# Kernel optimization log

Hardware: AMD Instinct MI355X
Metric: run time of the kernel (lower is better)

## Reference

```python
import jax, jax.numpy as jnp
import numpy as np

C = 1.0      # base manifold curvature (Lorentz c)
C_E = 1.0    # expert manifold curvature (all experts init to c=1.0)
K = 1        # n_activated_experts (top-k)
SCALE = 2.0  # LResNet scale for shared-expert combine
EPS = 1e-8


def _lorentz_swiglu(x, W1, W3, W2, c_mid, c_out, prescale):
    """LorentzExpert / LorentzFeedForward: SwiGLU on space coords with Lorentz time lift.
    x: [T, D] (full Lorentz vector). W1,W3: [I-1, D]; W2: [D-1, I]. Returns [T, D]."""
    if prescale:
        x = x * np.float32(np.sqrt(C_E / C))  # x * sqrt(c_expert / c)
    s1 = jax.nn.silu(x @ W1.T)                 # [T, I-1] w1(x, return_space=True)
    s3 = x @ W3.T                              # [T, I-1] w3(x, return_space=True)
    sp = s1 * s3                               # gated space part
    t = jnp.sqrt(jnp.clip((sp * sp).sum(-1, keepdims=True) + c_mid, EPS))
    h = jnp.concatenate([t, sp], axis=-1)      # [T, I] point on expert manifold
    o = h @ W2.T                               # [T, D-1] w2 space output
    ot = jnp.sqrt(jnp.clip((o * o).sum(-1, keepdims=True) + c_out, EPS))
    return jnp.concatenate([ot, o], axis=-1)   # [T, D] on base manifold


def setup_inputs() -> dict:
    key = jax.random.key(0)
    ks = jax.random.split(key, 9)
    T, D, E, I = 2048, 1024, 8, 1024
    x = jax.random.normal(ks[0], (T, D), jnp.float32)
    gate_w = jax.random.normal(ks[1], (E, D - 1), jnp.float32) / np.sqrt(D - 1)
    gate_b = jax.random.normal(ks[2], (E,), jnp.float32) * 0.01
    W1 = jax.random.normal(ks[3], (E, I - 1, D), jnp.float32) / np.sqrt(D)
    W3 = jax.random.normal(ks[4], (E, I - 1, D), jnp.float32) / np.sqrt(D)
    W2 = jax.random.normal(ks[5], (E, D - 1, I), jnp.float32) / np.sqrt(I)
    Ws1 = jax.random.normal(ks[6], (I - 1, D), jnp.float32) / np.sqrt(D)
    Ws3 = jax.random.normal(ks[7], (I - 1, D), jnp.float32) / np.sqrt(D)
    Ws2 = jax.random.normal(ks[8], (D - 1, I), jnp.float32) / np.sqrt(I)
    return {"x": x, "gate_w": gate_w, "gate_b": gate_b, "W1": W1, "W3": W3,
            "W2": W2, "Ws1": Ws1, "Ws3": Ws3, "Ws2": Ws2}


def reference(x, gate_w, gate_b, W1, W3, W2, Ws1, Ws3, Ws2):
    T, D = x.shape
    E = gate_w.shape[0]
    # ---- Gate (softmax scoring, n_groups == 1, route_scale == 1.0) ----
    logits = x[:, 1:] @ gate_w.T                                    # [T, E]
    scores = jax.nn.softmax(logits.astype(jnp.float32), axis=-1)
    biased = scores + gate_b                                        # bias only affects routing
    _, idx = jax.lax.top_k(biased, K)                               # [T, K]
    weights = jnp.take_along_axis(scores, idx, axis=-1).astype(x.dtype)  # [T, K]
    # dense per-token expert gate weights [T, E]
    oh = jax.nn.one_hot(idx, E, dtype=x.dtype)                      # [T, K, E]
    gw = (oh * weights[..., None]).sum(axis=1)                      # [T, E]
    # ---- y init: project(zeros) -> [sqrt(c), 0, ..., 0] ----
    y0 = jnp.concatenate([jnp.full((T, 1), np.sqrt(C), x.dtype),
                          jnp.zeros((T, D - 1), x.dtype)], axis=-1)
    # ---- routed experts (dense reference: every expert on every token, masked combine) ----
    e_out = jax.vmap(lambda w1, w3, w2: _lorentz_swiglu(x, w1, w3, w2, C_E, C, True))(W1, W3, W2)  # [E, T, D]
    y = y0 + jnp.einsum('te,etd->td', gw, e_out)
    # ---- shared expert (LorentzFeedForward, stays on base manifold) ----
    z = _lorentz_swiglu(x, Ws1, Ws3, Ws2, C, C, False)
    # ---- LResNet weighted sum: normalize (z + scale*y) back to manifold ----
    comb = z + SCALE * y
    li = (comb[:, 1:] ** 2).sum(-1, keepdims=True) - comb[:, :1] ** 2  # Lorentz inner <comb,comb>
    out = np.float32(np.sqrt(C)) * comb / jnp.sqrt(jnp.clip(jnp.abs(li), EPS))
    return out
```

## Files before the change

### kernel.cpp

```cpp
#include <hip/hip_runtime.h>

typedef __bf16 bf16;
typedef __attribute__((ext_vector_type(8))) __bf16 bf16x8;
typedef __attribute__((ext_vector_type(4))) float floatx4;

#define TOK 2048
#define DD  1024
#define NE  8
#define LDA 40

__device__ __forceinline__ uint4 pack_bf8(float4 a, float4 b) {
  union { bf16 h[8]; uint4 u; } p;
  p.h[0] = (bf16)a.x; p.h[1] = (bf16)a.y; p.h[2] = (bf16)a.z; p.h[3] = (bf16)a.w;
  p.h[4] = (bf16)b.x; p.h[5] = (bf16)b.y; p.h[6] = (bf16)b.z; p.h[7] = (bf16)b.w;
  return p.u;
}

__global__ __launch_bounds__(256) void gate_cvt_kernel(
    const float* __restrict__ x, const float* __restrict__ gate_w,
    const float* __restrict__ gate_b, bf16* __restrict__ x_bf,
    int* __restrict__ eidx, float* __restrict__ ewgt)
{
  const int t = blockIdx.x, tid = threadIdx.x;
  const float4 v = ((const float4*)(x + (size_t)t * DD))[tid];
  union { bf16 h[4]; uint2 u; } pk;
  pk.h[0] = (bf16)v.x; pk.h[1] = (bf16)v.y; pk.h[2] = (bf16)v.z; pk.h[3] = (bf16)v.w;
  ((uint2*)(x_bf + (size_t)t * DD))[tid] = pk.u;

  float acc[NE];
#pragma unroll
  for (int e = 0; e < NE; ++e) acc[e] = 0.f;
  const float vv[4] = {v.x, v.y, v.z, v.w};
#pragma unroll
  for (int i = 0; i < 4; ++i) {
    const int d = tid * 4 + i;
    if (d >= 1) {
#pragma unroll
      for (int e = 0; e < NE; ++e) acc[e] += vv[i] * gate_w[e * (DD - 1) + d - 1];
    }
  }
#pragma unroll
  for (int off = 32; off > 0; off >>= 1) {
#pragma unroll
    for (int e = 0; e < NE; ++e) acc[e] += __shfl_down(acc[e], off);
  }
  __shared__ float red[4][NE];
  const int wid = tid >> 6, lane = tid & 63;
  if (lane == 0) {
#pragma unroll
    for (int e = 0; e < NE; ++e) red[wid][e] = acc[e];
  }
  __syncthreads();
  if (tid == 0) {
    float lg[NE];
#pragma unroll
    for (int e = 0; e < NE; ++e) lg[e] = red[0][e] + red[1][e] + red[2][e] + red[3][e];
    float m = lg[0];
    for (int e = 1; e < NE; ++e) m = fmaxf(m, lg[e]);
    float ex[NE], s = 0.f;
    for (int e = 0; e < NE; ++e) { ex[e] = expf(lg[e] - m); s += ex[e]; }
    const float inv = 1.f / s;
    int best = 0; float bb = ex[0] * inv + gate_b[0];
    for (int e = 1; e < NE; ++e) {
      const float b = ex[e] * inv + gate_b[e];
      if (b > bb) { bb = b; best = e; }
    }
    eidx[t] = best;
    ewgt[t] = ex[best] * inv;
  }
}

__global__ __launch_bounds__(256) void route_kernel(
    const int* __restrict__ eidx, int* __restrict__ perm,
    int* __restrict__ pos_of, int* __restrict__ seg_base)
{
  __shared__ int cnt[NE], off[NE], bas[NE + 1];
  const int tid = threadIdx.x;
  if (tid < NE) cnt[tid] = 0;
  __syncthreads();
  for (int t = tid; t < TOK; t += 256) atomicAdd(&cnt[eidx[t]], 1);
  __syncthreads();
  if (tid == 0) {
    int run = 0;
    for (int e = 0; e < NE; ++e) { bas[e] = run; off[e] = run; run += cnt[e]; }
    bas[NE] = run;
  }
  __syncthreads();
  for (int t = tid; t < TOK; t += 256) {
    const int e = eidx[t];
    const int p = atomicAdd(&off[e], 1);
    perm[p] = t;
    pos_of[t] = p;
  }
  if (tid <= NE) seg_base[tid] = bas[tid];
}

__global__ __launch_bounds__(256) void mlp1_kernel(
    const bf16* __restrict__ x_bf,
    const float* __restrict__ W1, const float* __restrict__ W3,
    const float* __restrict__ Ws1, const float* __restrict__ Ws3,
    const int* __restrict__ perm, const int* __restrict__ seg_base,
    bf16* __restrict__ h_r, bf16* __restrict__ h_s,
    float* __restrict__ ss_r, float* __restrict__ ss_z)
{
  const int nt = blockIdx.x;
  const int mslot = blockIdx.y;
  const int tid = threadIdx.x;
  int base, cnt, row0;
  const float *w1p, *w3p;
  const int* permp;
  bf16* hbuf;
  float* ssbuf;
  if (mslot < 128) {
    const int e = mslot >> 4;
    base = seg_base[e];
    cnt  = seg_base[e + 1] - base;
    row0 = (mslot & 15) * 128;
    if (row0 >= cnt) return;
    w1p = W1 + (size_t)e * 1023 * 1024;
    w3p = W3 + (size_t)e * 1023 * 1024;
    permp = perm; hbuf = h_r; ssbuf = ss_r;
  } else {
    base = 0; cnt = TOK; row0 = (mslot - 128) * 128;
    w1p = Ws1; w3p = Ws3;
    permp = nullptr; hbuf = h_s; ssbuf = ss_z;
  }
  const int n0 = nt * 64;

  __shared__ __align__(16) bf16 As[128 * LDA];
  __shared__ __align__(16) bf16 B1s[64 * LDA];
  __shared__ __align__(16) bf16 B3s[64 * LDA];
  __shared__ int toks[128];

  if (tid < 128) {
    int r = row0 + tid;
    if (r >= cnt) r = cnt - 1;
    toks[tid] = permp ? permp[base + r] : r;
  }
  __syncthreads();

  const int arow = tid >> 1, acol = (tid & 1) * 16;
  const bf16* aptr = x_bf + (size_t)toks[arow] * DD + acol;
  bf16* const alds = As + arow * LDA + acol;

  const int brow = tid >> 2, bcol = (tid & 3) * 8;
  int bn = n0 + brow; if (bn > 1022) bn = 1022;
  const float* b1ptr = w1p + (size_t)bn * 1024 + bcol;
  const float* b3ptr = w3p + (size_t)bn * 1024 + bcol;
  bf16* const b1lds = B1s + brow * LDA + bcol;
  bf16* const b3lds = B3s + brow * LDA + bcol;

  const int wid = tid >> 6, lane = tid & 63;
  const int wr = (wid >> 1) * 64, wc = (wid & 1) * 32;
  const int lrow = lane & 15, quad = lane >> 4;

  const floatx4 fz = {0.f, 0.f, 0.f, 0.f};
  floatx4 acc1[4][2], acc3[4][2];
#pragma unroll
  for (int mi = 0; mi < 4; ++mi)
#pragma unroll
    for (int ni = 0; ni < 2; ++ni) { acc1[mi][ni] = fz; acc3[mi][ni] = fz; }

  uint4  a0  = *(const uint4*)(aptr);
  uint4  a1  = *(const uint4*)(aptr + 8);
  float4 f10 = *(const float4*)(b1ptr);
  float4 f11 = *(const float4*)(b1ptr + 4);
  float4 f30 = *(const float4*)(b3ptr);
  float4 f31 = *(const float4*)(b3ptr + 4);

  for (int k0 = 0; k0 < 1024; k0 += 32) {
    __syncthreads();
    *(uint4*)alds       = a0;
    *(uint4*)(alds + 8) = a1;
    *(uint4*)b1lds = pack_bf8(f10, f11);
    *(uint4*)b3lds = pack_bf8(f30, f31);
    __syncthreads();
    const int kn = (k0 + 32 < 1024) ? (k0 + 32) : 0;
    a0  = *(const uint4*)(aptr + kn);
    a1  = *(const uint4*)(aptr + kn + 8);
    f10 = *(const float4*)(b1ptr + kn);
    f11 = *(const float4*)(b1ptr + kn + 4);
    f30 = *(const float4*)(b3ptr + kn);
    f31 = *(const float4*)(b3ptr + kn + 4);

    bf16x8 af[4], b1f[2], b3f[2];
#pragma unroll
    for (int mi = 0; mi < 4; ++mi)
      af[mi] = *(const bf16x8*)(As + (wr + mi * 16 + lrow) * LDA + quad * 8);
#pragma unroll
    for (int ni = 0; ni < 2; ++ni) {
      b1f[ni] = *(const bf16x8*)(B1s + (wc + ni * 16 + lrow) * LDA + quad * 8);
      b3f[ni] = *(const bf16x8*)(B3s + (wc + ni * 16 + lrow) * LDA + quad * 8);
    }
#pragma unroll
    for (int mi = 0; mi < 4; ++mi)
#pragma unroll
      for (int ni = 0; ni < 2; ++ni) {
        acc1[mi][ni] = __builtin_amdgcn_mfma_f32_16x16x32_bf16(af[mi], b1f[ni], acc1[mi][ni], 0, 0, 0);
        acc3[mi][ni] = __builtin_amdgcn_mfma_f32_16x16x32_bf16(af[mi], b3f[ni], acc3[mi][ni], 0, 0, 0);
      }
  }

  const int mbase = base + row0;
#pragma unroll
  for (int mi = 0; mi < 4; ++mi) {
#pragma unroll
    for (int r = 0; r < 4; ++r) {
      const int row = wr + mi * 16 + quad * 4 + r;
      const bool rowok = (row0 + row) < cnt;
      float ssum = 0.f;
#pragma unroll
      for (int ni = 0; ni < 2; ++ni) {
        const float s1 = acc1[mi][ni][r];
        const float s3 = acc3[mi][ni][r];
        const float sp = (s1 / (1.f + __expf(-s1))) * s3;
        const int n = n0 + wc + ni * 16 + lrow;
        if (rowok && n < 1023) {
          hbuf[(size_t)(mbase + row) * 1024 + 1 + n] = (bf16)sp;
          ssum += sp * sp;
        }
      }
      ssum += __shfl_xor(ssum, 1);
      ssum += __shfl_xor(ssum, 2);
      ssum += __shfl_xor(ssum, 4);
      ssum += __shfl_xor(ssum, 8);
      if (lrow == 0 && rowok) atomicAdd(ssbuf + mbase + row, ssum);
    }
  }
}

__global__ __launch_bounds__(256) void finalize_t_kernel(
    const float* __restrict__ ss_r, const float* __restrict__ ss_z,
    bf16* __restrict__ h_r, bf16* __restrict__ h_s)
{
  const int i = blockIdx.x * 256 + threadIdx.x;
  if (i < TOK) {
    h_r[(size_t)i * 1024] = (bf16)sqrtf(ss_r[i] + 1.0f);
    h_s[(size_t)i * 1024] = (bf16)sqrtf(ss_z[i] + 1.0f);
  }
}

__global__ __launch_bounds__(256) void mlp2_kernel(
    const bf16* __restrict__ h_r, const bf16* __restrict__ h_s,
    const float* __restrict__ W2, const float* __restrict__ Ws2,
    const int* __restrict__ seg_base,
    float* __restrict__ o_r, float* __restrict__ o_s,
    float* __restrict__ ss_or, float* __restrict__ ss_oz)
{
  const int nt = blockIdx.x;
  const int mslot = blockIdx.y;
  const int tid = threadIdx.x;
  int base, cnt, row0;
  const float* wp;
  const bf16* abuf;
  float *obuf, *ssbuf;
  if (mslot < 128) {
    const int e = mslot >> 4;
    base = seg_base[e];
    cnt  = seg_base[e + 1] - base;
    row0 = (mslot & 15) * 128;
    if (row0 >= cnt) return;
    wp = W2 + (size_t)e * 1023 * 1024;
    abuf = h_r; obuf = o_r; ssbuf = ss_or;
  } else {
    base = 0; cnt = TOK; row0 = (mslot - 128) * 128;
    wp = Ws2; abuf = h_s; obuf = o_s; ssbuf = ss_oz;
  }
  const int n0 = nt * 128;

  __shared__ __align__(16) bf16 As[128 * LDA];
  __shared__ __align__(16) bf16 Bs[128 * LDA];

  const int arow = tid >> 1, acol = (tid & 1) * 16;
  int ar = row0 + arow; if (ar >= cnt) ar = cnt - 1;
  const bf16* aptr = abuf + (size_t)(base + ar) * 1024 + acol;
  bf16* const alds = As + arow * LDA + acol;

  const int brow = tid >> 1, bcol = (tid & 1) * 16;
  int bn = n0 + brow; if (bn > 1022) bn = 1022;
  const float* bptr = wp + (size_t)bn * 1024 + bcol;
  bf16* const blds = Bs + brow * LDA + bcol;

  const int wid = tid >> 6, lane = tid & 63;
  const int wr = (wid >> 1) * 64, wc = (wid & 1) * 64;
  const int lrow = lane & 15, quad = lane >> 4;

  const floatx4 fz = {0.f, 0.f, 0.f, 0.f};
  floatx4 acc[4][4];
#pragma unroll
  for (int mi = 0; mi < 4; ++mi)
#pragma unroll
    for (int ni = 0; ni < 4; ++ni) acc[mi][ni] = fz;

  uint4  a0 = *(const uint4*)(aptr);
  uint4  a1 = *(const uint4*)(aptr + 8);
  float4 f0 = *(const float4*)(bptr);
  float4 f1 = *(const float4*)(bptr + 4);
  float4 f2 = *(const float4*)(bptr + 8);
  float4 f3 = *(const float4*)(bptr + 12);

  for (int k0 = 0; k0 < 1024; k0 += 32) {
    __syncthreads();
    *(uint4*)alds       = a0;
    *(uint4*)(alds + 8) = a1;
    *(uint4*)blds       = pack_bf8(f0, f1);
    *(uint4*)(blds + 8) = pack_bf8(f2, f3);
    __syncthreads();
    const int kn = (k0 + 32 < 1024) ? (k0 + 32) : 0;
    a0 = *(const uint4*)(aptr + kn);
    a1 = *(const uint4*)(aptr + kn + 8);
    f0 = *(const float4*)(bptr + kn);
    f1 = *(const float4*)(bptr + kn + 4);
    f2 = *(const float4*)(bptr + kn + 8);
    f3 = *(const float4*)(bptr + kn + 12);

    bf16x8 af[4], bf_[4];
#pragma unroll
    for (int mi = 0; mi < 4; ++mi)
      af[mi] = *(const bf16x8*)(As + (wr + mi * 16 + lrow) * LDA + quad * 8);
#pragma unroll
    for (int ni = 0; ni < 4; ++ni)
      bf_[ni] = *(const bf16x8*)(Bs + (wc + ni * 16 + lrow) * LDA + quad * 8);
#pragma unroll
    for (int mi = 0; mi < 4; ++mi)
#pragma unroll
      for (int ni = 0; ni < 4; ++ni)
        acc[mi][ni] = __builtin_amdgcn_mfma_f32_16x16x32_bf16(af[mi], bf_[ni], acc[mi][ni], 0, 0, 0);
  }

  const int mbase = base + row0;
#pragma unroll
  for (int mi = 0; mi < 4; ++mi) {
#pragma unroll
    for (int r = 0; r < 4; ++r) {
      const int row = wr + mi * 16 + quad * 4 + r;
      const bool rowok = (row0 + row) < cnt;
      float ssum = 0.f;
#pragma unroll
      for (int ni = 0; ni < 4; ++ni) {
        const float v = acc[mi][ni][r];
        const int n = n0 + wc + ni * 16 + lrow;
        if (rowok && n < 1023) {
          obuf[(size_t)(mbase + row) * 1024 + n] = v;
          ssum += v * v;
        }
      }
      ssum += __shfl_xor(ssum, 1);
      ssum += __shfl_xor(ssum, 2);
      ssum += __shfl_xor(ssum, 4);
      ssum += __shfl_xor(ssum, 8);
      if (lrow == 0 && rowok) atomicAdd(ssbuf + mbase + row, ssum);
    }
  }
}

__global__ __launch_bounds__(256) void combine_kernel(
    const float* __restrict__ o_r, const float* __restrict__ o_s,
    const float* __restrict__ ss_or, const float* __restrict__ ss_oz,
    const int* __restrict__ pos_of, const float* __restrict__ wgt,
    float* __restrict__ out)
{
  const int t = blockIdx.x, tid = threadIdx.x;
  const int p = pos_of[t];
  const float w = wgt[t];
  const float4 oz = ((const float4*)(o_s + (size_t)t * 1024))[tid];
  const float4 oe = ((const float4*)(o_r + (size_t)p * 1024))[tid];
  const float tw = 2.f * w;
  float c0 = oz.x + tw * oe.x;
  float c1 = oz.y + tw * oe.y;
  float c2 = oz.z + tw * oe.z;
  float c3 = (tid == 255) ? 0.f : (oz.w + tw * oe.w);
  float ssum = c0 * c0 + c1 * c1 + c2 * c2 + c3 * c3;
#pragma unroll
  for (int off = 32; off > 0; off >>= 1) ssum += __shfl_down(ssum, off);
  __shared__ float rs[4];
  if ((tid & 63) == 0) rs[tid >> 6] = ssum;
  __syncthreads();
  const float space2 = rs[0] + rs[1] + rs[2] + rs[3];
  const float comb0 = sqrtf(ss_oz[t] + 1.f) + 2.f + 2.f * w * sqrtf(ss_or[p] + 1.f);
  const float li = space2 - comb0 * comb0;
  const float inv = 1.f / sqrtf(fmaxf(fabsf(li), 1e-8f));
  float* orow = out + (size_t)t * 1024;
  const int j = 1 + tid * 4;
  orow[j]     = c0 * inv;
  orow[j + 1] = c1 * inv;
  orow[j + 2] = c2 * inv;
  if (tid != 255) orow[j + 3] = c3 * inv;
  if (tid == 0) orow[0] = comb0 * inv;
}

extern "C" void kernel_launch(void* const* d_in, const int* in_sizes, int n_in,
                              void* d_out, int out_size, void* d_ws, size_t ws_size,
                              hipStream_t stream) {
  const float* x      = (const float*)d_in[0];
  const float* gate_w = (const float*)d_in[1];
  const float* gate_b = (const float*)d_in[2];
  const float* W1     = (const float*)d_in[3];
  const float* W3     = (const float*)d_in[4];
  const float* W2     = (const float*)d_in[5];
  const float* Ws1    = (const float*)d_in[6];
  const float* Ws3    = (const float*)d_in[7];
  const float* Ws2    = (const float*)d_in[8];
  float* out = (float*)d_out;

  char* ws = (char*)d_ws;
  size_t off = 0;
  auto alloc = [&](size_t bytes) {
    void* p = ws + off;
    off += (bytes + 255) & ~(size_t)255;
    return p;
  };
  bf16*  x_bf = (bf16*) alloc((size_t)TOK * 1024 * 2);
  bf16*  h_r  = (bf16*) alloc((size_t)TOK * 1024 * 2);
  bf16*  h_s  = (bf16*) alloc((size_t)TOK * 1024 * 2);
  float* o_r  = (float*)alloc((size_t)TOK * 1024 * 4);
  float* o_s  = (float*)alloc((size_t)TOK * 1024 * 4);
  float* ss   = (float*)alloc((size_t)4 * TOK * 4);
  int*   eidx = (int*)  alloc((size_t)TOK * 4);
  float* ewgt = (float*)alloc((size_t)TOK * 4);
  int*   perm = (int*)  alloc((size_t)TOK * 4);
  int*   posf = (int*)  alloc((size_t)TOK * 4);
  int*   segb = (int*)  alloc(64);

  float* ss_r  = ss;
  float* ss_z  = ss + TOK;
  float* ss_or = ss + 2 * TOK;
  float* ss_oz = ss + 3 * TOK;

  hipMemsetAsync(ss, 0, (size_t)4 * TOK * 4, stream);
  gate_cvt_kernel<<<TOK, 256, 0, stream>>>(x, gate_w, gate_b, x_bf, eidx, ewgt);
  route_kernel<<<1, 256, 0, stream>>>(eidx, perm, posf, segb);
  mlp1_kernel<<<dim3(16, 144), 256, 0, stream>>>(x_bf, W1, W3, Ws1, Ws3, perm, segb,
                                                 h_r, h_s, ss_r, ss_z);
  finalize_t_kernel<<<8, 256, 0, stream>>>(ss_r, ss_z, h_r, h_s);
  mlp2_kernel<<<dim3(8, 144), 256, 0, stream>>>(h_r, h_s, W2, Ws2, segb,
                                                o_r, o_s, ss_or, ss_oz);
  combine_kernel<<<TOK, 256, 0, stream>>>(o_r, o_s, ss_or, ss_oz, posf, ewgt, out);
}
```

Measured before the change: 278.6 us.

## Build compact per-expert work list and shrink GEMM tiles to 64 rows

New measurement: 285.1 us. +2.3%, slower.

```diff
diff --git a/kernel.cpp b/kernel.cpp
--- a/kernel.cpp
+++ b/kernel.cpp
@@ -8,6 +8,7 @@
 #define DD  1024
 #define NE  8
 #define LDA 40
+#define MAXSLOT 72
 
 __device__ __forceinline__ uint4 pack_bf8(float4 a, float4 b) {
   union { bf16 h[8]; uint4 u; } p;
@@ -72,7 +73,7 @@
 
 __global__ __launch_bounds__(256) void route_kernel(
     const int* __restrict__ eidx, int* __restrict__ perm,
-    int* __restrict__ pos_of, int* __restrict__ seg_base)
+    int* __restrict__ pos_of, int4* __restrict__ wl, int* __restrict__ wl_n)
 {
   __shared__ int cnt[NE], off[NE], bas[NE + 1];
   const int tid = threadIdx.x;
@@ -84,6 +85,14 @@
     int run = 0;
     for (int e = 0; e < NE; ++e) { bas[e] = run; off[e] = run; run += cnt[e]; }
     bas[NE] = run;
+    int n = 0;
+    for (int e = 0; e < NE; ++e)
+      for (int r0 = 0; r0 < cnt[e]; r0 += 64) {
+        int rows = cnt[e] - r0; if (rows > 64) rows = 64;
+        wl[n++] = make_int4(bas[e] + r0, rows, e, 0);
+      }
+    for (int r0 = 0; r0 < TOK; r0 += 64) wl[n++] = make_int4(r0, 64, NE, 0);
+    *wl_n = n;
   }
   __syncthreads();
   for (int t = tid; t < TOK; t += 256) {
@@ -92,54 +101,42 @@
     perm[p] = t;
     pos_of[t] = p;
   }
-  if (tid <= NE) seg_base[tid] = bas[tid];
 }
 
 __global__ __launch_bounds__(256) void mlp1_kernel(
     const bf16* __restrict__ x_bf,
     const float* __restrict__ W1, const float* __restrict__ W3,
     const float* __restrict__ Ws1, const float* __restrict__ Ws3,
-    const int* __restrict__ perm, const int* __restrict__ seg_base,
+    const int* __restrict__ perm, const int4* __restrict__ wl,
+    const int* __restrict__ wl_n,
     bf16* __restrict__ h_r, bf16* __restrict__ h_s,
     float* __restrict__ ss_r, float* __restrict__ ss_z)
 {
-  const int nt = blockIdx.x;
-  const int mslot = blockIdx.y;
+  const int bid = blockIdx.x;
+  const int slot = bid >> 4, nt = bid & 15;
+  if (slot >= *wl_n) return;
+  const int4 wle = wl[slot];
+  const int mbase = wle.x, rows = wle.y, eid = wle.z;
   const int tid = threadIdx.x;
-  int base, cnt, row0;
-  const float *w1p, *w3p;
-  const int* permp;
-  bf16* hbuf;
-  float* ssbuf;
-  if (mslot < 128) {
-    const int e = mslot >> 4;
-    base = seg_base[e];
-    cnt  = seg_base[e + 1] - base;
-    row0 = (mslot & 15) * 128;
-    if (row0 >= cnt) return;
-    w1p = W1 + (size_t)e * 1023 * 1024;
-    w3p = W3 + (size_t)e * 1023 * 1024;
-    permp = perm; hbuf = h_r; ssbuf = ss_r;
-  } else {
-    base = 0; cnt = TOK; row0 = (mslot - 128) * 128;
-    w1p = Ws1; w3p = Ws3;
-    permp = nullptr; hbuf = h_s; ssbuf = ss_z;
-  }
+  const bool routed = (eid < NE);
+  const float* w1p = routed ? W1 + (size_t)eid * 1023 * 1024 : Ws1;
+  const float* w3p = routed ? W3 + (size_t)eid * 1023 * 1024 : Ws3;
+  bf16* hbuf  = routed ? h_r : h_s;
+  float* ssbuf = routed ? ss_r : ss_z;
   const int n0 = nt * 64;
 
-  __shared__ __align__(16) bf16 As[128 * LDA];
+  __shared__ __align__(16) bf16 As[64 * LDA];
   __shared__ __align__(16) bf16 B1s[64 * LDA];
   __shared__ __align__(16) bf16 B3s[64 * LDA];
-  __shared__ int toks[128];
-
-  if (tid < 128) {
-    int r = row0 + tid;
-    if (r >= cnt) r = cnt - 1;
-    toks[tid] = permp ? permp[base + r] : r;
-  }
-  __syncthreads();
-
-  const int arow = tid >> 1, acol = (tid & 1) * 16;
+  __shared__ int toks[64];
+
+  if (tid < 64) {
+    int r = tid < rows ? tid : rows - 1;
+    toks[tid] = routed ? perm[mbase + r] : (mbase + r);
+  }
+  __syncthreads();
+
+  const int arow = tid >> 2, acol = (tid & 3) * 8;
   const bf16* aptr = x_bf + (size_t)toks[arow] * DD + acol;
   bf16* const alds = As + arow * LDA + acol;
 
@@ -151,18 +148,15 @@
   bf16* const b3lds = B3s + brow * LDA + bcol;
 
   const int wid = tid >> 6, lane = tid & 63;
-  const int wr = (wid >> 1) * 64, wc = (wid & 1) * 32;
+  const int wc = wid * 16;
   const int lrow = lane & 15, quad = lane >> 4;
 
   const floatx4 fz = {0.f, 0.f, 0.f, 0.f};
-  floatx4 acc1[4][2], acc3[4][2];
-#pragma unroll
-  for (int mi = 0; mi < 4; ++mi)
-#pragma unroll
-    for (int ni = 0; ni < 2; ++ni) { acc1[mi][ni] = fz; acc3[mi][ni] = fz; }
+  floatx4 acc1[4], acc3[4];
+#pragma unroll
+  for (int mi = 0; mi < 4; ++mi) { acc1[mi] = fz; acc3[mi] = fz; }
 
   uint4  a0  = *(const uint4*)(aptr);
-  uint4  a1  = *(const uint4*)(aptr + 8);
   float4 f10 = *(const float4*)(b1ptr);
   float4 f11 = *(const float4*)(b1ptr + 4);
   float4 f30 = *(const float4*)(b3ptr);
@@ -170,61 +164,47 @@
 
   for (int k0 = 0; k0 < 1024; k0 += 32) {
     __syncthreads();
-    *(uint4*)alds       = a0;
-    *(uint4*)(alds + 8) = a1;
+    *(uint4*)alds  = a0;
     *(uint4*)b1lds = pack_bf8(f10, f11);
     *(uint4*)b3lds = pack_bf8(f30, f31);
     __syncthreads();
     const int kn = (k0 + 32 < 1024) ? (k0 + 32) : 0;
     a0  = *(const uint4*)(aptr + kn);
-    a1  = *(const uint4*)(aptr + kn + 8);
     f10 = *(const float4*)(b1ptr + kn);
     f11 = *(const float4*)(b1ptr + kn + 4);
     f30 = *(const float4*)(b3ptr + kn);
     f31 = *(const float4*)(b3ptr + kn + 4);
 
-    bf16x8 af[4], b1f[2], b3f[2];
+    bf16x8 af[4], b1f, b3f;
 #pragma unroll
     for (int mi = 0; mi < 4; ++mi)
-      af[mi] = *(const bf16x8*)(As + (wr + mi * 16 + lrow) * LDA + quad * 8);
-#pragma unroll
-    for (int ni = 0; ni < 2; ++ni) {
-      b1f[ni] = *(const bf16x8*)(B1s + (wc + ni * 16 + lrow) * LDA + quad * 8);
-      b3f[ni] = *(const bf16x8*)(B3s + (wc + ni * 16 + lrow) * LDA + quad * 8);
-    }
-#pragma unroll
-    for (int mi = 0; mi < 4; ++mi)
-#pragma unroll
-      for (int ni = 0; ni < 2; ++ni) {
-        acc1[mi][ni] = __builtin_amdgcn_mfma_f32_16x16x32_bf16(af[mi], b1f[ni], acc1[mi][ni], 0, 0, 0);
-        acc3[mi][ni] = __builtin_amdgcn_mfma_f32_16x16x32_bf16(af[mi], b3f[ni], acc3[mi][ni], 0, 0, 0);
-      }
-  }
-
-  const int mbase = base + row0;
+      af[mi] = *(const bf16x8*)(As + (mi * 16 + lrow) * LDA + quad * 8);
+    b1f = *(const bf16x8*)(B1s + (wc + lrow) * LDA + quad * 8);
+    b3f = *(const bf16x8*)(B3s + (wc + lrow) * LDA + quad * 8);
+#pragma unroll
+    for (int mi = 0; mi < 4; ++mi) {
+      acc1[mi] = __builtin_amdgcn_mfma_f32_16x16x32_bf16(af[mi], b1f, acc1[mi], 0, 0, 0);
+      acc3[mi] = __builtin_amdgcn_mfma_f32_16x16x32_bf16(af[mi], b3f, acc3[mi], 0, 0, 0);
+    }
+  }
+
+  const int n = n0 + wc + lrow;
 #pragma unroll
   for (int mi = 0; mi < 4; ++mi) {
 #pragma unroll
     for (int r = 0; r < 4; ++r) {
-      const int row = wr + mi * 16 + quad * 4 + r;
-      const bool rowok = (row0 + row) < cnt;
-      float ssum = 0.f;
-#pragma unroll
-      for (int ni = 0; ni < 2; ++ni) {
-        const float s1 = acc1[mi][ni][r];
-        const float s3 = acc3[mi][ni][r];
-        const float sp = (s1 / (1.f + __expf(-s1))) * s3;
-        const int n = n0 + wc + ni * 16 + lrow;
-        if (rowok && n < 1023) {
-          hbuf[(size_t)(mbase + row) * 1024 + 1 + n] = (bf16)sp;
-          ssum += sp * sp;
-        }
-      }
+      const int row = mi * 16 + quad * 4 + r;
+      const bool ok = (row < rows) && (n < 1023);
+      const float s1 = acc1[mi][r];
+      const float s3 = acc3[mi][r];
+      const float sp = (s1 / (1.f + __expf(-s1))) * s3;
+      float ssum = ok ? sp * sp : 0.f;
+      if (ok) hbuf[(size_t)(mbase + row) * 1024 + 1 + n] = (bf16)sp;
       ssum += __shfl_xor(ssum, 1);
       ssum += __shfl_xor(ssum, 2);
       ssum += __shfl_xor(ssum, 4);
       ssum += __shfl_xor(ssum, 8);
-      if (lrow == 0 && rowok) atomicAdd(ssbuf + mbase + row, ssum);
+      if (lrow == 0 && row < rows) atomicAdd(ssbuf + mbase + row, ssum);
     }
   }
 }
@@ -243,113 +223,84 @@
 __global__ __launch_bounds__(256) void mlp2_kernel(
     const bf16* __restrict__ h_r, const bf16* __restrict__ h_s,
     const float* __restrict__ W2, const float* __restrict__ Ws2,
-    const int* __restrict__ seg_base,
+    const int4* __restrict__ wl, const int* __restrict__ wl_n,
     float* __restrict__ o_r, float* __restrict__ o_s,
     float* __restrict__ ss_or, float* __restrict__ ss_oz)
 {
-  const int nt = blockIdx.x;
-  const int mslot = blockIdx.y;
+  const int bid = blockIdx.x;
+  const int slot = bid >> 4, nt = bid & 15;
+  if (slot >= *wl_n) return;
+  const int4 wle = wl[slot];
+  const int mbase = wle.x, rows = wle.y, eid = wle.z;
   const int tid = threadIdx.x;
-  int base, cnt, row0;
-  const float* wp;
-  const bf16* abuf;
-  float *obuf, *ssbuf;
-  if (mslot < 128) {
-    const int e = mslot >> 4;
-    base = seg_base[e];
-    cnt  = seg_base[e + 1] - base;
-    row0 = (mslot & 15) * 128;
-    if (row0 >= cnt) return;
-    wp = W2 + (size_t)e * 1023 * 1024;
-    abuf = h_r; obuf = o_r; ssbuf = ss_or;
-  } else {
-    base = 0; cnt = TOK; row0 = (mslot - 128) * 128;
-    wp = Ws2; abuf = h_s; obuf = o_s; ssbuf = ss_oz;
-  }
-  const int n0 = nt * 128;
-
-  __shared__ __align__(16) bf16 As[128 * LDA];
-  __shared__ __align__(16) bf16 Bs[128 * LDA];
-
-  const int arow = tid >> 1, acol = (tid & 1) * 16;
-  int ar = row0 + arow; if (ar >= cnt) ar = cnt - 1;
-  const bf16* aptr = abuf + (size_t)(base + ar) * 1024 + acol;
+  const bool routed = (eid < NE);
+  const float* wp = routed ? W2 + (size_t)eid * 1023 * 1024 : Ws2;
+  const bf16* abuf = routed ? h_r : h_s;
+  float* obuf  = routed ? o_r : o_s;
+  float* ssbuf = routed ? ss_or : ss_oz;
+  const int n0 = nt * 64;
+
+  __shared__ __align__(16) bf16 As[64 * LDA];
+  __shared__ __align__(16) bf16 Bs[64 * LDA];
+
+  const int arow = tid >> 2, acol = (tid & 3) * 8;
+  const int ar = arow < rows ? arow : rows - 1;
+  const bf16* aptr = abuf + (size_t)(mbase + ar) * 1024 + acol;
   bf16* const alds = As + arow * LDA + acol;
 
-  const int brow = tid >> 1, bcol = (tid & 1) * 16;
+  const int brow = tid >> 2, bcol = (tid & 3) * 8;
   int bn = n0 + brow; if (bn > 1022) bn = 1022;
   const float* bptr = wp + (size_t)bn * 1024 + bcol;
   bf16* const blds = Bs + brow * LDA + bcol;
 
   const int wid = tid >> 6, lane = tid & 63;
-  const int wr = (wid >> 1) * 64, wc = (wid & 1) * 64;
+  const int wc = wid * 16;
   const int lrow = lane & 15, quad = lane >> 4;
 
   const floatx4 fz = {0.f, 0.f, 0.f, 0.f};
-  floatx4 acc[4][4];
-#pragma unroll
-  for (int mi = 0; mi < 4; ++mi)
-#pragma unroll
-    for (int ni = 0; ni < 4; ++ni) acc[mi][ni] = fz;
+  floatx4 acc[4];
+#pragma unroll
+  for (int mi = 0; mi < 4; ++mi) acc[mi] = fz;
 
   uint4  a0 = *(const uint4*)(aptr);
-  uint4  a1 = *(const uint4*)(aptr + 8);
   float4 f0 = *(const float4*)(bptr);
   float4 f1 = *(const float4*)(bptr + 4);
-  float4 f2 = *(const float4*)(bptr + 8);
-  float4 f3 = *(const float4*)(bptr + 12);
 
   for (int k0 = 0; k0 < 1024; k0 += 32) {
     __syncthreads();
-    *(uint4*)alds       = a0;
-    *(uint4*)(alds + 8) = a1;
-    *(uint4*)blds       = pack_bf8(f0, f1);
-    *(uint4*)(blds + 8) = pack_bf8(f2, f3);
+    *(uint4*)alds = a0;
+    *(uint4*)blds = pack_bf8(f0, f1);
     __syncthreads();
     const int kn = (k0 + 32 < 1024) ? (k0 + 32) : 0;
     a0 = *(const uint4*)(aptr + kn);
-    a1 = *(const uint4*)(aptr + kn + 8);
     f0 = *(const float4*)(bptr + kn);
     f1 = *(const float4*)(bptr + kn + 4);
-    f2 = *(const float4*)(bptr + kn + 8);
-    f3 = *(const float4*)(bptr + kn + 12);
-
-    bf16x8 af[4], bf_[4];
+
+    bf16x8 af[4], bfr;
 #pragma unroll
     for (int mi = 0; mi < 4; ++mi)
-      af[mi] = *(const bf16x8*)(As + (wr + mi * 16 + lrow) * LDA + quad * 8);
-#pragma unroll
-    for (int ni = 0; ni < 4; ++ni)
-      bf_[ni] = *(const bf16x8*)(Bs + (wc + ni * 16 + lrow) * LDA + quad * 8);
+      af[mi] = *(const bf16x8*)(As + (mi * 16 + lrow) * LDA + quad * 8);
+    bfr = *(const bf16x8*)(Bs + (wc + lrow) * LDA + quad * 8);
 #pragma unroll
     for (int mi = 0; mi < 4; ++mi)
-#pragma unroll
-      for (int ni = 0; ni < 4; ++ni)
-        acc[mi][ni] = __builtin_amdgcn_mfma_f32_16x16x32_bf16(af[mi], bf_[ni], acc[mi][ni], 0, 0, 0);
-  }
-
-  const int mbase = base + row0;
+      acc[mi] = __builtin_amdgcn_mfma_f32_16x16x32_bf16(af[mi], bfr, acc[mi], 0, 0, 0);
+  }
+
+  const int n = n0 + wc + lrow;
 #pragma unroll
   for (int mi = 0; mi < 4; ++mi) {
 #pragma unroll
     for (int r = 0; r < 4; ++r) {
-      const int row = wr + mi * 16 + quad * 4 + r;
-      const bool rowok = (row0 + row) < cnt;
-      float ssum = 0.f;
-#pragma unroll
-      for (int ni = 0; ni < 4; ++ni) {
-        const float v = acc[mi][ni][r];
-        const int n = n0 + wc + ni * 16 + lrow;
-        if (rowok && n < 1023) {
-          obuf[(size_t)(mbase + row) * 1024 + n] = v;
-          ssum += v * v;
-        }
-      }
+      const int row = mi * 16 + quad * 4 + r;
+      const bool ok = (row < rows) && (n < 1023);
+      const float v = acc[mi][r];
+      float ssum = ok ? v * v : 0.f;
+      if (ok) obuf[(size_t)(mbase + row) * 1024 + n] = v;
       ssum += __shfl_xor(ssum, 1);
       ssum += __shfl_xor(ssum, 2);
       ssum += __shfl_xor(ssum, 4);
       ssum += __shfl_xor(ssum, 8);
-      if (lrow == 0 && rowok) atomicAdd(ssbuf + mbase + row, ssum);
+      if (lrow == 0 && row < rows) atomicAdd(ssbuf + mbase + row, ssum);
     }
   }
 }
@@ -420,7 +371,8 @@
   float* ewgt = (float*)alloc((size_t)TOK * 4);
   int*   perm = (int*)  alloc((size_t)TOK * 4);
   int*   posf = (int*)  alloc((size_t)TOK * 4);
-  int*   segb = (int*)  alloc(64);
+  int4*  wl   = (int4*) alloc((size_t)MAXSLOT * 16);
+  int*   wln  = (int*)  alloc(16);
 
   float* ss_r  = ss;
   float* ss_z  = ss + TOK;
@@ -429,11 +381,11 @@
 
   hipMemsetAsync(ss, 0, (size_t)4 * TOK * 4, stream);
   gate_cvt_kernel<<<TOK, 256, 0, stream>>>(x, gate_w, gate_b, x_bf, eidx, ewgt);
-  route_kernel<<<1, 256, 0, stream>>>(eidx, perm, posf, segb);
-  mlp1_kernel<<<dim3(16, 144), 256, 0, stream>>>(x_bf, W1, W3, Ws1, Ws3, perm, segb,
-                                                 h_r, h_s, ss_r, ss_z);
+  route_kernel<<<1, 256, 0, stream>>>(eidx, perm, posf, wl, wln);
+  mlp1_kernel<<<MAXSLOT * 16, 256, 0, stream>>>(x_bf, W1, W3, Ws1, Ws3, perm, wl, wln,
+                                                h_r, h_s, ss_r, ss_z);
   finalize_t_kernel<<<8, 256, 0, stream>>>(ss_r, ss_z, h_r, h_s);
-  mlp2_kernel<<<dim3(8, 144), 256, 0, stream>>>(h_r, h_s, W2, Ws2, segb,
+  mlp2_kernel<<<MAXSLOT * 16, 256, 0, stream>>>(h_r, h_s, W2, Ws2, wl, wln,
                                                 o_r, o_s, ss_or, ss_oz);
   combine_kernel<<<TOK, 256, 0, stream>>>(o_r, o_s, ss_or, ss_oz, posf, ewgt, out);
 }
```
